# Kernel optimization log

Hardware: AMD Instinct MI355X
Metric: run time of the kernel (lower is better)

Reference implementation:

```python
import jax, jax.numpy as jnp
import numpy as np

W_NBITS = 8
A_NBITS = 8


def _fake_quant_weight_per_channel(w, nbits):
    # symmetric per-output-channel (row) fake quantization
    qmax = float(2 ** (nbits - 1) - 1)
    scale = jnp.max(jnp.abs(w), axis=1, keepdims=True) / qmax  # [out, 1]
    scale = jnp.maximum(scale, 1e-8)
    return jnp.clip(jnp.round(w / scale), -qmax - 1.0, qmax) * scale


def _fake_quant_act_per_group(x, group_size, nbits):
    # dynamic symmetric per-group fake quantization along the feature dim
    qmax = float(2 ** (nbits - 1) - 1)
    tokens, feat = x.shape
    xg = x.reshape(tokens, feat // group_size, group_size)
    scale = jnp.max(jnp.abs(xg), axis=-1, keepdims=True) / qmax  # [T, G, 1]
    scale = jnp.maximum(scale, 1e-8)
    xq = jnp.clip(jnp.round(xg / scale), -qmax - 1.0, qmax) * scale
    return xq.reshape(tokens, feat)


def setup_inputs() -> dict:
    key = jax.random.key(0)
    k1, k2, k3 = jax.random.split(key, 3)
    tokens, in_f, out_f = 8192, 4096, 4096
    x = jax.random.normal(k1, (tokens, in_f), dtype=jnp.float32)
    weight = jax.random.normal(k2, (out_f, in_f), dtype=jnp.float32) * 0.02
    bias = jax.random.normal(k3, (out_f,), dtype=jnp.float32) * 0.02
    return {"x": x, "weight": weight, "bias": bias, "group_size": 128}


def reference(x, weight, bias, group_size):
    w_q = _fake_quant_weight_per_channel(weight, W_NBITS)
    x_q = _fake_quant_act_per_group(x, group_size, A_NBITS)
    # F.linear: x @ w.T + b
    return jnp.einsum("tc,oc->to", x_q, w_q) + bias
```

## Files before the change

### kernel.cpp

```cpp
#include <hip/hip_runtime.h>
#include <stdint.h>


typedef __attribute__((ext_vector_type(4))) int   i32x4;
typedef __attribute__((ext_vector_type(4))) float f32x4;

static __device__ __forceinline__ void load_lds16(const void* g, void* l) {
    __builtin_amdgcn_global_load_lds(
        (const __attribute__((address_space(1))) void*)g,
        (__attribute__((address_space(3))) void*)l, 16, 0, 0);
}

static __device__ __forceinline__ int8_t q8m(float v, float inv) {
    float q = rintf(v * inv);
    q = fminf(fmaxf(q, -128.0f), 127.0f);
    return (int8_t)(int)q;
}

__global__ __launch_bounds__(256) void quant_act_kernel(
        const float* __restrict__ x, int8_t* __restrict__ xq,
        float* __restrict__ sxT, int M) {
    const int row = blockIdx.x, t = threadIdx.x;
    const float* xr = x + (size_t)row * 4096;
    float4 v[4];
#pragma unroll
    for (int i = 0; i < 4; i++)
        v[i] = *(const float4*)(xr + t * 16 + i * 4);
    float m = 0.0f;
#pragma unroll
    for (int i = 0; i < 4; i++)
        m = fmaxf(m, fmaxf(fmaxf(fabsf(v[i].x), fabsf(v[i].y)),
                           fmaxf(fabsf(v[i].z), fabsf(v[i].w))));
    m = fmaxf(m, __shfl_xor(m, 1));
    m = fmaxf(m, __shfl_xor(m, 2));
    m = fmaxf(m, __shfl_xor(m, 4));
    const float scale = fmaxf(m / 127.0f, 1e-8f);
    const float inv = 1.0f / scale;
    union { int8_t b[16]; i32x4 w; } o;
#pragma unroll
    for (int i = 0; i < 4; i++) {
        o.b[i * 4 + 0] = q8m(v[i].x, inv);
        o.b[i * 4 + 1] = q8m(v[i].y, inv);
        o.b[i * 4 + 2] = q8m(v[i].z, inv);
        o.b[i * 4 + 3] = q8m(v[i].w, inv);
    }
    *(i32x4*)(xq + (size_t)row * 4096 + t * 16) = o.w;
    if ((t & 7) == 0)
        sxT[(size_t)(t >> 3) * M + row] = scale;
}

__global__ __launch_bounds__(256) void quant_wgt_kernel(
        const float* __restrict__ w, int8_t* __restrict__ wq,
        float* __restrict__ sw) {
    const int row = blockIdx.x, t = threadIdx.x;
    const float* wr = w + (size_t)row * 4096;
    float4 v[4];
#pragma unroll
    for (int i = 0; i < 4; i++)
        v[i] = *(const float4*)(wr + t * 16 + i * 4);
    float m = 0.0f;
#pragma unroll
    for (int i = 0; i < 4; i++)
        m = fmaxf(m, fmaxf(fmaxf(fabsf(v[i].x), fabsf(v[i].y)),
                           fmaxf(fabsf(v[i].z), fabsf(v[i].w))));
#pragma unroll
    for (int off = 1; off < 64; off <<= 1)
        m = fmaxf(m, __shfl_xor(m, off));
    __shared__ float wm[4];
    if ((t & 63) == 0) wm[t >> 6] = m;
    __syncthreads();
    m = fmaxf(fmaxf(wm[0], wm[1]), fmaxf(wm[2], wm[3]));
    const float scale = fmaxf(m / 127.0f, 1e-8f);
    if (t == 0) sw[row] = scale;
    const float inv = 1.0f / scale;
    union { int8_t b[16]; i32x4 w4; } o;
#pragma unroll
    for (int i = 0; i < 4; i++) {
        o.b[i * 4 + 0] = q8m(v[i].x, inv);
        o.b[i * 4 + 1] = q8m(v[i].y, inv);
        o.b[i * 4 + 2] = q8m(v[i].z, inv);
        o.b[i * 4 + 3] = q8m(v[i].w, inv);
    }
    *(i32x4*)(wq + (size_t)row * 4096 + t * 16) = o.w4;
}

__global__ __launch_bounds__(256, 2) void gemm_i8_kernel(
        const int8_t* __restrict__ A, const int8_t* __restrict__ B,
        const float* __restrict__ sxT, const float* __restrict__ sw,
        const float* __restrict__ bias, float* __restrict__ C,
        int M, int N, int K) {
    __shared__ __align__(16) int8_t As[128 * 128];
    __shared__ __align__(16) int8_t Bs[128 * 128];
    const int tid = threadIdx.x;
    const int wave = tid >> 6, lane = tid & 63;
    const int bm = blockIdx.y * 128, bn = blockIdx.x * 128;
    const int wm = (wave >> 1) * 64, wn = (wave & 1) * 64;

    f32x4 acc[4][4];
#pragma unroll
    for (int i = 0; i < 4; i++)
#pragma unroll
        for (int j = 0; j < 4; j++) acc[i][j] = (f32x4){0.f, 0.f, 0.f, 0.f};

    const int srow = wave * 8 + (lane >> 3);
    const int scol = (((lane & 7) ^ ((lane >> 3) & 7)) * 16);
    const size_t sK = (size_t)K;
    const int8_t* Ag = A + (size_t)(bm + srow) * sK + scol;
    const int8_t* Bg = B + (size_t)(bn + srow) * sK + scol;
    int8_t* AsW = As + (wave * 8) * 128;
    int8_t* BsW = Bs + (wave * 8) * 128;

    const int fr = lane & 15, q = lane >> 4, r7 = lane & 7;
    const float* sxg = sxT + bm + wm + q * 4;

    for (int k0 = 0; k0 < K; k0 += 128) {
#pragma unroll
        for (int i = 0; i < 4; i++) {
            load_lds16(Ag + k0 + (size_t)i * 32 * sK, AsW + i * 32 * 128);
            load_lds16(Bg + k0 + (size_t)i * 32 * sK, BsW + i * 32 * 128);
        }
        f32x4 sxv[4];
#pragma unroll
        for (int mi = 0; mi < 4; mi++)
            sxv[mi] = *(const f32x4*)(sxg + (size_t)(k0 >> 7) * M + mi * 16);
        __syncthreads();

        i32x4 a[4][2], b[4][2];
#pragma unroll
        for (int mi = 0; mi < 4; mi++) {
            const int arow = wm + mi * 16 + fr;
            const int brow = wn + mi * 16 + fr;
#pragma unroll
            for (int h = 0; h < 2; h++) {
                a[mi][h] = *(const i32x4*)(As + arow * 128 +
                                           ((h * 4 + q) ^ r7) * 16);
                b[mi][h] = *(const i32x4*)(Bs + brow * 128 +
                                           ((h * 4 + q) ^ r7) * 16);
            }
        }
#pragma unroll
        for (int mi = 0; mi < 4; mi++)
#pragma unroll
            for (int ni = 0; ni < 4; ni++) {
                i32x4 iacc = __builtin_amdgcn_mfma_i32_16x16x64_i8(
                    a[mi][0], b[ni][0], (i32x4){0, 0, 0, 0}, 0, 0, 0);
                iacc = __builtin_amdgcn_mfma_i32_16x16x64_i8(
                    a[mi][1], b[ni][1], iacc, 0, 0, 0);
#pragma unroll
                for (int r = 0; r < 4; r++)
                    acc[mi][ni][r] += (float)iacc[r] * sxv[mi][r];
            }
        __syncthreads();
    }

    const int or0 = bm + wm + q * 4;
    const int oc0 = bn + wn + fr;
    float swv[4], bv[4];
#pragma unroll
    for (int ni = 0; ni < 4; ni++) {
        swv[ni] = sw[oc0 + ni * 16];
        bv[ni] = bias[oc0 + ni * 16];
    }
#pragma unroll
    for (int mi = 0; mi < 4; mi++)
#pragma unroll
        for (int ni = 0; ni < 4; ni++)
#pragma unroll
            for (int r = 0; r < 4; r++)
                C[(size_t)(or0 + mi * 16 + r) * N + (oc0 + ni * 16)] =
                    acc[mi][ni][r] * swv[ni] + bv[ni];
}

extern "C" void kernel_launch(void* const* d_in, const int* in_sizes, int n_in,
                              void* d_out, int out_size, void* d_ws, size_t ws_size,
                              hipStream_t stream) {
    const float* x    = (const float*)d_in[0];
    const float* w    = (const float*)d_in[1];
    const float* bias = (const float*)d_in[2];

    const int out_f  = in_sizes[2];
    const int in_f   = in_sizes[1] / out_f;
    const int tokens = in_sizes[0] / in_f;
    const int G = in_f / 128;

    int8_t* xq  = (int8_t*)d_ws;
    int8_t* wq  = xq + (size_t)tokens * in_f;
    float*  sxT = (float*)(wq + (size_t)out_f * in_f);
    float*  sw  = sxT + (size_t)G * tokens;
    float*  out = (float*)d_out;

    quant_act_kernel<<<tokens, 256, 0, stream>>>(x, xq, sxT, tokens);
    quant_wgt_kernel<<<out_f, 256, 0, stream>>>(w, wq, sw);

    dim3 grid(out_f / 128, tokens / 128);
    gemm_i8_kernel<<<grid, 256, 0, stream>>>(xq, wq, sxT, sw, bias, out,
                                             tokens, out_f, in_f);
}
```

Before: 445.8 us.

## Enlarge GEMM tile to 256x256 with double-buffered LDS ping-pong pipeline

Moves the int8 GEMM from 128x128 tiles with 4 waves to 256x256 tiles with 8 waves. The LDS tile buffers are double-buffered, and the global-to-LDS loads for the next K step are interleaved between four MFMA quadrants using explicit barriers, waitcnt and setprio. The workgroup index is remapped with an XCD-aware swizzle. The aim is to hide load latency and raise operand reuse. In exchange it uses 128KB of LDS per block, which limits occupancy, and it depends on fragile manual synchronisation.

```diff
diff --git a/kernel.cpp b/kernel.cpp
--- a/kernel.cpp
+++ b/kernel.cpp
@@ -84,74 +84,139 @@
     *(i32x4*)(wq + (size_t)row * 4096 + t * 16) = o.w4;
 }
 
-__global__ __launch_bounds__(256, 2) void gemm_i8_kernel(
+#define QUAD(mh, nh)                                                         \
+    _Pragma("unroll")                                                        \
+    for (int mi2 = 0; mi2 < 4; ++mi2) {                                      \
+        _Pragma("unroll")                                                    \
+        for (int nj = 0; nj < 2; ++nj) {                                     \
+            const int ni = (nh) * 2 + nj;                                    \
+            i32x4 t = __builtin_amdgcn_mfma_i32_16x16x64_i8(                 \
+                a[mi2][0], b[ni][0], (i32x4){0, 0, 0, 0}, 0, 0, 0);          \
+            t = __builtin_amdgcn_mfma_i32_16x16x64_i8(                       \
+                a[mi2][1], b[ni][1], t, 0, 0, 0);                            \
+            _Pragma("unroll")                                                \
+            for (int r = 0; r < 4; ++r)                                      \
+                acc[(mh) * 4 + mi2][ni][r] += (float)t[r] * sxv[mi2][r];     \
+        }                                                                    \
+    }
+
+__global__ __launch_bounds__(512, 2) void gemm_i8_kernel(
         const int8_t* __restrict__ A, const int8_t* __restrict__ B,
         const float* __restrict__ sxT, const float* __restrict__ sw,
         const float* __restrict__ bias, float* __restrict__ C,
         int M, int N, int K) {
-    __shared__ __align__(16) int8_t As[128 * 128];
-    __shared__ __align__(16) int8_t Bs[128 * 128];
+    __shared__ __align__(16) int8_t As[2][256 * 128];
+    __shared__ __align__(16) int8_t Bs[2][256 * 128];
     const int tid = threadIdx.x;
     const int wave = tid >> 6, lane = tid & 63;
-    const int bm = blockIdx.y * 128, bn = blockIdx.x * 128;
-    const int wm = (wave >> 1) * 64, wn = (wave & 1) * 64;
-
-    f32x4 acc[4][4];
-#pragma unroll
-    for (int i = 0; i < 4; i++)
-#pragma unroll
-        for (int j = 0; j < 4; j++) acc[i][j] = (f32x4){0.f, 0.f, 0.f, 0.f};
+
+    const int nwg = gridDim.x, nN = N >> 8;
+    const int wg = ((int)blockIdx.x & 7) * (nwg >> 3) + ((int)blockIdx.x >> 3);
+    const int bm = (wg / nN) << 8, bn = (wg % nN) << 8;
+
+    const int wm = (wave >> 2) << 7, wn = (wave & 3) << 6;
+    const int fr = lane & 15, q = lane >> 4, r7 = lane & 7;
 
     const int srow = wave * 8 + (lane >> 3);
-    const int scol = (((lane & 7) ^ ((lane >> 3) & 7)) * 16);
+    const int scol = ((lane & 7) ^ ((lane >> 3) & 7)) << 4;
     const size_t sK = (size_t)K;
     const int8_t* Ag = A + (size_t)(bm + srow) * sK + scol;
     const int8_t* Bg = B + (size_t)(bn + srow) * sK + scol;
-    int8_t* AsW = As + (wave * 8) * 128;
-    int8_t* BsW = Bs + (wave * 8) * 128;
-
-    const int fr = lane & 15, q = lane >> 4, r7 = lane & 7;
-    const float* sxg = sxT + bm + wm + q * 4;
-
-    for (int k0 = 0; k0 < K; k0 += 128) {
-#pragma unroll
-        for (int i = 0; i < 4; i++) {
-            load_lds16(Ag + k0 + (size_t)i * 32 * sK, AsW + i * 32 * 128);
-            load_lds16(Bg + k0 + (size_t)i * 32 * sK, BsW + i * 32 * 128);
+    const int sldsw = wave * 8 * 128;
+
+    f32x4 acc[8][4];
+#pragma unroll
+    for (int i = 0; i < 8; i++)
+#pragma unroll
+        for (int jn = 0; jn < 4; jn++) acc[i][jn] = (f32x4){0.f, 0.f, 0.f, 0.f};
+
+    const int abase = (wm + fr) * 128;
+    const int bbase = (wn + fr) * 128;
+    const int c0 = (q ^ r7) << 4, c1 = ((4 + q) ^ r7) << 4;
+    const float* sxw = sxT + bm + wm + q * 4;
+
+    const int NT = K >> 7;
+
+    load_lds16(Bg,             &Bs[0][sldsw]);
+    load_lds16(Bg +  64 * sK,  &Bs[0][ 64 * 128 + sldsw]);
+    load_lds16(Bg + 128 * sK,  &Bs[0][128 * 128 + sldsw]);
+    load_lds16(Bg + 192 * sK,  &Bs[0][192 * 128 + sldsw]);
+    load_lds16(Ag,             &As[0][sldsw]);
+    load_lds16(Ag + 128 * sK,  &As[0][128 * 128 + sldsw]);
+    load_lds16(Ag +  64 * sK,  &As[0][ 64 * 128 + sldsw]);
+    load_lds16(Ag + 192 * sK,  &As[0][192 * 128 + sldsw]);
+    asm volatile("s_waitcnt vmcnt(2)" ::: "memory");
+    __builtin_amdgcn_s_barrier();
+
+    for (int j = 0; j < NT; ++j) {
+        const int cur = j & 1, nxt = cur ^ 1;
+        const size_t kn = (size_t)((j + 1 < NT) ? j + 1 : j) << 7;
+        const int8_t* Ac = As[cur];
+        const int8_t* Bc = Bs[cur];
+        const float* sxg = sxw + (size_t)j * M;
+
+        i32x4 a[4][2], b[4][2];
+        f32x4 sxv[4];
+
+#pragma unroll
+        for (int i = 0; i < 4; ++i) {
+            a[i][0] = *(const i32x4*)(Ac + abase + i * 2048 + c0);
+            a[i][1] = *(const i32x4*)(Ac + abase + i * 2048 + c1);
+            b[i][0] = *(const i32x4*)(Bc + bbase + i * 2048 + c0);
+            b[i][1] = *(const i32x4*)(Bc + bbase + i * 2048 + c1);
         }
-        f32x4 sxv[4];
-#pragma unroll
-        for (int mi = 0; mi < 4; mi++)
-            sxv[mi] = *(const f32x4*)(sxg + (size_t)(k0 >> 7) * M + mi * 16);
-        __syncthreads();
-
-        i32x4 a[4][2], b[4][2];
-#pragma unroll
-        for (int mi = 0; mi < 4; mi++) {
-            const int arow = wm + mi * 16 + fr;
-            const int brow = wn + mi * 16 + fr;
-#pragma unroll
-            for (int h = 0; h < 2; h++) {
-                a[mi][h] = *(const i32x4*)(As + arow * 128 +
-                                           ((h * 4 + q) ^ r7) * 16);
-                b[mi][h] = *(const i32x4*)(Bs + brow * 128 +
-                                           ((h * 4 + q) ^ r7) * 16);
-            }
+#pragma unroll
+        for (int i = 0; i < 4; ++i)
+            sxv[i] = *(const f32x4*)(sxg + i * 16);
+        load_lds16(Bg + kn,            &Bs[nxt][sldsw]);
+        load_lds16(Bg + kn + 64 * sK,  &Bs[nxt][64 * 128 + sldsw]);
+        __builtin_amdgcn_s_barrier();
+        asm volatile("s_waitcnt lgkmcnt(0)" ::: "memory");
+        __builtin_amdgcn_sched_barrier(0);
+        __builtin_amdgcn_s_setprio(1);
+        QUAD(0, 0)
+        __builtin_amdgcn_s_setprio(0);
+        __builtin_amdgcn_s_barrier();
+
+        load_lds16(Bg + kn + 128 * sK, &Bs[nxt][128 * 128 + sldsw]);
+        load_lds16(Bg + kn + 192 * sK, &Bs[nxt][192 * 128 + sldsw]);
+        __builtin_amdgcn_s_barrier();
+        __builtin_amdgcn_sched_barrier(0);
+        __builtin_amdgcn_s_setprio(1);
+        QUAD(0, 1)
+        __builtin_amdgcn_s_setprio(0);
+        asm volatile("s_waitcnt vmcnt(4)" ::: "memory");
+        __builtin_amdgcn_s_barrier();
+
+#pragma unroll
+        for (int i = 0; i < 4; ++i) {
+            a[i][0] = *(const i32x4*)(Ac + abase + 64 * 128 + i * 2048 + c0);
+            a[i][1] = *(const i32x4*)(Ac + abase + 64 * 128 + i * 2048 + c1);
         }
 #pragma unroll
-        for (int mi = 0; mi < 4; mi++)
-#pragma unroll
-            for (int ni = 0; ni < 4; ni++) {
-                i32x4 iacc = __builtin_amdgcn_mfma_i32_16x16x64_i8(
-                    a[mi][0], b[ni][0], (i32x4){0, 0, 0, 0}, 0, 0, 0);
-                iacc = __builtin_amdgcn_mfma_i32_16x16x64_i8(
-                    a[mi][1], b[ni][1], iacc, 0, 0, 0);
-#pragma unroll
-                for (int r = 0; r < 4; r++)
-                    acc[mi][ni][r] += (float)iacc[r] * sxv[mi][r];
-            }
-        __syncthreads();
-    }
+        for (int i = 0; i < 4; ++i)
+            sxv[i] = *(const f32x4*)(sxg + 64 + i * 16);
+        load_lds16(Ag + kn,            &As[nxt][sldsw]);
+        load_lds16(Ag + kn + 128 * sK, &As[nxt][128 * 128 + sldsw]);
+        __builtin_amdgcn_s_barrier();
+        asm volatile("s_waitcnt lgkmcnt(0)" ::: "memory");
+        __builtin_amdgcn_sched_barrier(0);
+        __builtin_amdgcn_s_setprio(1);
+        QUAD(1, 0)
+        __builtin_amdgcn_s_setprio(0);
+        __builtin_amdgcn_s_barrier();
+
+        load_lds16(Ag + kn + 64 * sK,  &As[nxt][64 * 128 + sldsw]);
+        load_lds16(Ag + kn + 192 * sK, &As[nxt][192 * 128 + sldsw]);
+        __builtin_amdgcn_s_barrier();
+        __builtin_amdgcn_sched_barrier(0);
+        __builtin_amdgcn_s_setprio(1);
+        QUAD(1, 1)
+        __builtin_amdgcn_s_setprio(0);
+        asm volatile("s_waitcnt vmcnt(2)" ::: "memory");
+        __builtin_amdgcn_s_barrier();
+    }
+    asm volatile("s_waitcnt vmcnt(0)" ::: "memory");
 
     const int or0 = bm + wm + q * 4;
     const int oc0 = bn + wn + fr;
@@ -162,7 +227,7 @@
         bv[ni] = bias[oc0 + ni * 16];
     }
 #pragma unroll
-    for (int mi = 0; mi < 4; mi++)
+    for (int mi = 0; mi < 8; mi++)
 #pragma unroll
         for (int ni = 0; ni < 4; ni++)
 #pragma unroll
@@ -192,7 +257,7 @@
     quant_act_kernel<<<tokens, 256, 0, stream>>>(x, xq, sxT, tokens);
     quant_wgt_kernel<<<out_f, 256, 0, stream>>>(w, wq, sw);
 
-    dim3 grid(out_f / 128, tokens / 128);
-    gemm_i8_kernel<<<grid, 256, 0, stream>>>(xq, wq, sxT, sw, bias, out,
-                                             tokens, out_f, in_f);
-}
+    const int nwg = (tokens / 256) * (out_f / 256);
+    gemm_i8_kernel<<<nwg, 512, 0, stream>>>(xq, wq, sxT, sw, bias, out,
+                                            tokens, out_f, in_f);
+}
```

After: 475.4 us. 6.6% more time.

## Double-buffer LDS tiles with single barrier and XCD-aware block remap

Applied to the files above, without the earlier changes.

Switches the int8 GEMM to double-buffered LDS so the next K tile's global-to-LDS loads are issued while MFMAs run on the current tile. This cuts the loop to one barrier per iteration, guarded by an explicit vmcnt wait. It also replaces the 2D grid with a 1D grid remapped so consecutive blocks on the same XCD share tiles, aiming for better L2 reuse. Activation scales are prefetched one tile ahead into alternating registers. The cost is doubled LDS (64KB per block), which may hurt two-blocks-per-CU occupancy, and the loop assumes an even tile count.

```diff
diff --git a/kernel.cpp b/kernel.cpp
--- a/kernel.cpp
+++ b/kernel.cpp
@@ -84,74 +84,106 @@
     *(i32x4*)(wq + (size_t)row * 4096 + t * 16) = o.w4;
 }
 
+#define ITER(CUR, SXC, SXN, J)                                               \
+    {                                                                        \
+        asm volatile("s_waitcnt vmcnt(0)" ::: "memory");                     \
+        __builtin_amdgcn_s_barrier();                                        \
+        const int jn = ((J) + 1 < NT) ? (J) + 1 : (J);                       \
+        const size_t kn = (size_t)jn << 7;                                   \
+        load_lds16(Ag + kn,            &As[(CUR) ^ 1][sldsw]);               \
+        load_lds16(Ag + kn + 32 * sK,  &As[(CUR) ^ 1][32 * 128 + sldsw]);    \
+        load_lds16(Ag + kn + 64 * sK,  &As[(CUR) ^ 1][64 * 128 + sldsw]);    \
+        load_lds16(Ag + kn + 96 * sK,  &As[(CUR) ^ 1][96 * 128 + sldsw]);    \
+        load_lds16(Bg + kn,            &Bs[(CUR) ^ 1][sldsw]);               \
+        load_lds16(Bg + kn + 32 * sK,  &Bs[(CUR) ^ 1][32 * 128 + sldsw]);    \
+        load_lds16(Bg + kn + 64 * sK,  &Bs[(CUR) ^ 1][64 * 128 + sldsw]);    \
+        load_lds16(Bg + kn + 96 * sK,  &Bs[(CUR) ^ 1][96 * 128 + sldsw]);    \
+        _Pragma("unroll")                                                    \
+        for (int mi = 0; mi < 4; ++mi)                                       \
+            SXN[mi] = *(const f32x4*)(sxg + (size_t)jn * M + mi * 16);       \
+        i32x4 a[4][2], b[4][2];                                              \
+        _Pragma("unroll")                                                    \
+        for (int mi = 0; mi < 4; ++mi) {                                     \
+            const int arow = wm + mi * 16 + fr;                              \
+            const int brow = wn + mi * 16 + fr;                              \
+            _Pragma("unroll")                                                \
+            for (int h = 0; h < 2; ++h) {                                    \
+                a[mi][h] = *(const i32x4*)(As[CUR] + arow * 128 +            \
+                                           (((h * 4 + q) ^ r7) << 4));       \
+                b[mi][h] = *(const i32x4*)(Bs[CUR] + brow * 128 +            \
+                                           (((h * 4 + q) ^ r7) << 4));       \
+            }                                                                \
+        }                                                                    \
+        __builtin_amdgcn_sched_barrier(0);                                   \
+        _Pragma("unroll")                                                    \
+        for (int ni = 0; ni < 4; ++ni) {                                     \
+            i32x4 it[4];                                                     \
+            _Pragma("unroll")                                                \
+            for (int mi = 0; mi < 4; ++mi) {                                 \
+                it[mi] = __builtin_amdgcn_mfma_i32_16x16x64_i8(              \
+                    a[mi][0], b[ni][0], (i32x4){0, 0, 0, 0}, 0, 0, 0);       \
+                it[mi] = __builtin_amdgcn_mfma_i32_16x16x64_i8(              \
+                    a[mi][1], b[ni][1], it[mi], 0, 0, 0);                    \
+            }                                                                \
+            _Pragma("unroll")                                                \
+            for (int mi = 0; mi < 4; ++mi)                                   \
+                _Pragma("unroll")                                            \
+                for (int r = 0; r < 4; ++r)                                  \
+                    acc[mi][ni][r] += (float)it[mi][r] * SXC[mi][r];         \
+        }                                                                    \
+    }
+
 __global__ __launch_bounds__(256, 2) void gemm_i8_kernel(
         const int8_t* __restrict__ A, const int8_t* __restrict__ B,
         const float* __restrict__ sxT, const float* __restrict__ sw,
         const float* __restrict__ bias, float* __restrict__ C,
         int M, int N, int K) {
-    __shared__ __align__(16) int8_t As[128 * 128];
-    __shared__ __align__(16) int8_t Bs[128 * 128];
+    __shared__ __align__(16) int8_t As[2][128 * 128];
+    __shared__ __align__(16) int8_t Bs[2][128 * 128];
     const int tid = threadIdx.x;
     const int wave = tid >> 6, lane = tid & 63;
-    const int bm = blockIdx.y * 128, bn = blockIdx.x * 128;
-    const int wm = (wave >> 1) * 64, wn = (wave & 1) * 64;
-
-    f32x4 acc[4][4];
-#pragma unroll
-    for (int i = 0; i < 4; i++)
-#pragma unroll
-        for (int j = 0; j < 4; j++) acc[i][j] = (f32x4){0.f, 0.f, 0.f, 0.f};
+
+    const int nwg = gridDim.x, nN = N >> 7;
+    const int wg = ((int)blockIdx.x & 7) * (nwg >> 3) + ((int)blockIdx.x >> 3);
+    const int bm = (wg / nN) << 7, bn = (wg % nN) << 7;
+
+    const int wm = (wave >> 1) << 6, wn = (wave & 1) << 6;
+    const int fr = lane & 15, q = lane >> 4, r7 = lane & 7;
 
     const int srow = wave * 8 + (lane >> 3);
-    const int scol = (((lane & 7) ^ ((lane >> 3) & 7)) * 16);
+    const int scol = ((lane & 7) ^ ((lane >> 3) & 7)) << 4;
     const size_t sK = (size_t)K;
     const int8_t* Ag = A + (size_t)(bm + srow) * sK + scol;
     const int8_t* Bg = B + (size_t)(bn + srow) * sK + scol;
-    int8_t* AsW = As + (wave * 8) * 128;
-    int8_t* BsW = Bs + (wave * 8) * 128;
-
-    const int fr = lane & 15, q = lane >> 4, r7 = lane & 7;
+    const int sldsw = wave * 8 * 128;
+
+    f32x4 acc[4][4];
+#pragma unroll
+    for (int i = 0; i < 4; i++)
+#pragma unroll
+        for (int jn2 = 0; jn2 < 4; jn2++) acc[i][jn2] = (f32x4){0.f, 0.f, 0.f, 0.f};
+
     const float* sxg = sxT + bm + wm + q * 4;
-
-    for (int k0 = 0; k0 < K; k0 += 128) {
-#pragma unroll
-        for (int i = 0; i < 4; i++) {
-            load_lds16(Ag + k0 + (size_t)i * 32 * sK, AsW + i * 32 * 128);
-            load_lds16(Bg + k0 + (size_t)i * 32 * sK, BsW + i * 32 * 128);
-        }
-        f32x4 sxv[4];
-#pragma unroll
-        for (int mi = 0; mi < 4; mi++)
-            sxv[mi] = *(const f32x4*)(sxg + (size_t)(k0 >> 7) * M + mi * 16);
-        __syncthreads();
-
-        i32x4 a[4][2], b[4][2];
-#pragma unroll
-        for (int mi = 0; mi < 4; mi++) {
-            const int arow = wm + mi * 16 + fr;
-            const int brow = wn + mi * 16 + fr;
-#pragma unroll
-            for (int h = 0; h < 2; h++) {
-                a[mi][h] = *(const i32x4*)(As + arow * 128 +
-                                           ((h * 4 + q) ^ r7) * 16);
-                b[mi][h] = *(const i32x4*)(Bs + brow * 128 +
-                                           ((h * 4 + q) ^ r7) * 16);
-            }
-        }
-#pragma unroll
-        for (int mi = 0; mi < 4; mi++)
-#pragma unroll
-            for (int ni = 0; ni < 4; ni++) {
-                i32x4 iacc = __builtin_amdgcn_mfma_i32_16x16x64_i8(
-                    a[mi][0], b[ni][0], (i32x4){0, 0, 0, 0}, 0, 0, 0);
-                iacc = __builtin_amdgcn_mfma_i32_16x16x64_i8(
-                    a[mi][1], b[ni][1], iacc, 0, 0, 0);
-#pragma unroll
-                for (int r = 0; r < 4; r++)
-                    acc[mi][ni][r] += (float)iacc[r] * sxv[mi][r];
-            }
-        __syncthreads();
-    }
+    const int NT = K >> 7;
+
+    load_lds16(Ag,            &As[0][sldsw]);
+    load_lds16(Ag + 32 * sK,  &As[0][32 * 128 + sldsw]);
+    load_lds16(Ag + 64 * sK,  &As[0][64 * 128 + sldsw]);
+    load_lds16(Ag + 96 * sK,  &As[0][96 * 128 + sldsw]);
+    load_lds16(Bg,            &Bs[0][sldsw]);
+    load_lds16(Bg + 32 * sK,  &Bs[0][32 * 128 + sldsw]);
+    load_lds16(Bg + 64 * sK,  &Bs[0][64 * 128 + sldsw]);
+    load_lds16(Bg + 96 * sK,  &Bs[0][96 * 128 + sldsw]);
+    f32x4 sxa[4], sxb[4];
+#pragma unroll
+    for (int mi = 0; mi < 4; ++mi)
+        sxa[mi] = *(const f32x4*)(sxg + mi * 16);
+
+    for (int j = 0; j < NT; j += 2) {
+        ITER(0, sxa, sxb, j)
+        ITER(1, sxb, sxa, j + 1)
+    }
+    asm volatile("s_waitcnt vmcnt(0)" ::: "memory");
 
     const int or0 = bm + wm + q * 4;
     const int oc0 = bn + wn + fr;
@@ -192,7 +224,7 @@
     quant_act_kernel<<<tokens, 256, 0, stream>>>(x, xq, sxT, tokens);
     quant_wgt_kernel<<<out_f, 256, 0, stream>>>(w, wq, sw);
 
-    dim3 grid(out_f / 128, tokens / 128);
-    gemm_i8_kernel<<<grid, 256, 0, stream>>>(xq, wq, sxT, sw, bias, out,
-                                             tokens, out_f, in_f);
-}
+    const int nwg = (tokens / 128) * (out_f / 128);
+    gemm_i8_kernel<<<nwg, 256, 0, stream>>>(xq, wq, sxT, sw, bias, out,
+                                            tokens, out_f, in_f);
+}
```

After: 560.3 us. +25.7%, slower.

## Enlarge GEMM tile to 256 tokens and swap operands for vectorized stores

Applied to the files above, without the earlier changes.

The int8 GEMM block tile grows from 128x128 to 128 outputs by 256 tokens, with each wave computing a 64x128 sub-tile. Weights become the MFMA A operand and activations the B operand, so accumulator rows map to output channels. That lets the epilogue store with float4 writes and load scales and bias as vectors. The larger tile raises arithmetic intensity per LDS load, in exchange for twice the accumulator registers and 48KB of LDS, which may cut occupancy below two blocks per CU.

```diff
diff --git a/kernel.cpp b/kernel.cpp
--- a/kernel.cpp
+++ b/kernel.cpp
@@ -85,90 +85,107 @@
 }
 
 __global__ __launch_bounds__(256, 2) void gemm_i8_kernel(
-        const int8_t* __restrict__ A, const int8_t* __restrict__ B,
+        const int8_t* __restrict__ Xq, const int8_t* __restrict__ Wq,
         const float* __restrict__ sxT, const float* __restrict__ sw,
         const float* __restrict__ bias, float* __restrict__ C,
         int M, int N, int K) {
-    __shared__ __align__(16) int8_t As[128 * 128];
-    __shared__ __align__(16) int8_t Bs[128 * 128];
+    __shared__ __align__(16) int8_t Ws[128 * 128];
+    __shared__ __align__(16) int8_t Xs[256 * 128];
     const int tid = threadIdx.x;
     const int wave = tid >> 6, lane = tid & 63;
-    const int bm = blockIdx.y * 128, bn = blockIdx.x * 128;
-    const int wm = (wave >> 1) * 64, wn = (wave & 1) * 64;
-
-    f32x4 acc[4][4];
-#pragma unroll
-    for (int i = 0; i < 4; i++)
-#pragma unroll
-        for (int j = 0; j < 4; j++) acc[i][j] = (f32x4){0.f, 0.f, 0.f, 0.f};
+    const int bo = blockIdx.x * 128;
+    const int bt = blockIdx.y * 256;
+    const int wo = (wave & 1) << 6, wt = (wave >> 1) << 7;
+    const int fr = lane & 15, q = lane >> 4, r7 = lane & 7;
 
     const int srow = wave * 8 + (lane >> 3);
-    const int scol = (((lane & 7) ^ ((lane >> 3) & 7)) * 16);
+    const int scol = ((lane & 7) ^ ((lane >> 3) & 7)) << 4;
     const size_t sK = (size_t)K;
-    const int8_t* Ag = A + (size_t)(bm + srow) * sK + scol;
-    const int8_t* Bg = B + (size_t)(bn + srow) * sK + scol;
-    int8_t* AsW = As + (wave * 8) * 128;
-    int8_t* BsW = Bs + (wave * 8) * 128;
-
-    const int fr = lane & 15, q = lane >> 4, r7 = lane & 7;
-    const float* sxg = sxT + bm + wm + q * 4;
-
-    for (int k0 = 0; k0 < K; k0 += 128) {
-#pragma unroll
-        for (int i = 0; i < 4; i++) {
-            load_lds16(Ag + k0 + (size_t)i * 32 * sK, AsW + i * 32 * 128);
-            load_lds16(Bg + k0 + (size_t)i * 32 * sK, BsW + i * 32 * 128);
+    const int8_t* Wg = Wq + (size_t)(bo + srow) * sK + scol;
+    const int8_t* Xg = Xq + (size_t)(bt + srow) * sK + scol;
+    const int sldsw = wave * 8 * 128;
+
+    f32x4 facc[4][8];
+#pragma unroll
+    for (int i = 0; i < 4; i++)
+#pragma unroll
+        for (int jn = 0; jn < 8; jn++) facc[i][jn] = (f32x4){0.f, 0.f, 0.f, 0.f};
+
+    const float* sxb = sxT + bt + wt + fr;
+    const int NT = K >> 7;
+
+    for (int j = 0; j < NT; ++j) {
+        const size_t k0 = (size_t)j << 7;
+#pragma unroll
+        for (int i = 0; i < 4; ++i)
+            load_lds16(Wg + k0 + (size_t)i * 32 * sK, Ws + i * 32 * 128 + sldsw);
+#pragma unroll
+        for (int i = 0; i < 8; ++i)
+            load_lds16(Xg + k0 + (size_t)i * 32 * sK, Xs + i * 32 * 128 + sldsw);
+        float sxs[8];
+#pragma unroll
+        for (int ni = 0; ni < 8; ++ni)
+            sxs[ni] = sxb[(size_t)j * M + ni * 16];
+        __syncthreads();
+
+        i32x4 a[4][2];
+#pragma unroll
+        for (int mi = 0; mi < 4; ++mi) {
+            const int arow = (wo + mi * 16 + fr) * 128;
+#pragma unroll
+            for (int h = 0; h < 2; ++h)
+                a[mi][h] = *(const i32x4*)(Ws + arow + (((h * 4 + q) ^ r7) << 4));
         }
-        f32x4 sxv[4];
-#pragma unroll
-        for (int mi = 0; mi < 4; mi++)
-            sxv[mi] = *(const f32x4*)(sxg + (size_t)(k0 >> 7) * M + mi * 16);
-        __syncthreads();
-
-        i32x4 a[4][2], b[4][2];
-#pragma unroll
-        for (int mi = 0; mi < 4; mi++) {
-            const int arow = wm + mi * 16 + fr;
-            const int brow = wn + mi * 16 + fr;
-#pragma unroll
-            for (int h = 0; h < 2; h++) {
-                a[mi][h] = *(const i32x4*)(As + arow * 128 +
-                                           ((h * 4 + q) ^ r7) * 16);
-                b[mi][h] = *(const i32x4*)(Bs + brow * 128 +
-                                           ((h * 4 + q) ^ r7) * 16);
+#pragma unroll
+        for (int half = 0; half < 2; ++half) {
+            i32x4 b[4][2];
+#pragma unroll
+            for (int nj = 0; nj < 4; ++nj) {
+                const int brow = (wt + (half * 4 + nj) * 16 + fr) * 128;
+#pragma unroll
+                for (int h = 0; h < 2; ++h)
+                    b[nj][h] = *(const i32x4*)(Xs + brow +
+                                               (((h * 4 + q) ^ r7) << 4));
+            }
+#pragma unroll
+            for (int nj = 0; nj < 4; ++nj) {
+                const float s = sxs[half * 4 + nj];
+                i32x4 it[4];
+#pragma unroll
+                for (int mi = 0; mi < 4; ++mi) {
+                    it[mi] = __builtin_amdgcn_mfma_i32_16x16x64_i8(
+                        a[mi][0], b[nj][0], (i32x4){0, 0, 0, 0}, 0, 0, 0);
+                    it[mi] = __builtin_amdgcn_mfma_i32_16x16x64_i8(
+                        a[mi][1], b[nj][1], it[mi], 0, 0, 0);
+                }
+#pragma unroll
+                for (int mi = 0; mi < 4; ++mi)
+#pragma unroll
+                    for (int r = 0; r < 4; ++r)
+                        facc[mi][half * 4 + nj][r] += (float)it[mi][r] * s;
             }
         }
-#pragma unroll
-        for (int mi = 0; mi < 4; mi++)
-#pragma unroll
-            for (int ni = 0; ni < 4; ni++) {
-                i32x4 iacc = __builtin_amdgcn_mfma_i32_16x16x64_i8(
-                    a[mi][0], b[ni][0], (i32x4){0, 0, 0, 0}, 0, 0, 0);
-                iacc = __builtin_amdgcn_mfma_i32_16x16x64_i8(
-                    a[mi][1], b[ni][1], iacc, 0, 0, 0);
-#pragma unroll
-                for (int r = 0; r < 4; r++)
-                    acc[mi][ni][r] += (float)iacc[r] * sxv[mi][r];
-            }
         __syncthreads();
     }
 
-    const int or0 = bm + wm + q * 4;
-    const int oc0 = bn + wn + fr;
-    float swv[4], bv[4];
-#pragma unroll
-    for (int ni = 0; ni < 4; ni++) {
-        swv[ni] = sw[oc0 + ni * 16];
-        bv[ni] = bias[oc0 + ni * 16];
-    }
-#pragma unroll
-    for (int mi = 0; mi < 4; mi++)
-#pragma unroll
-        for (int ni = 0; ni < 4; ni++)
-#pragma unroll
-            for (int r = 0; r < 4; r++)
-                C[(size_t)(or0 + mi * 16 + r) * N + (oc0 + ni * 16)] =
-                    acc[mi][ni][r] * swv[ni] + bv[ni];
+    const int o4 = bo + wo + q * 4;
+    f32x4 swv[4], bv[4];
+#pragma unroll
+    for (int mi = 0; mi < 4; ++mi) {
+        swv[mi] = *(const f32x4*)(sw + o4 + mi * 16);
+        bv[mi]  = *(const f32x4*)(bias + o4 + mi * 16);
+    }
+#pragma unroll
+    for (int mi = 0; mi < 4; ++mi)
+#pragma unroll
+        for (int ni = 0; ni < 8; ++ni) {
+            f32x4 o;
+#pragma unroll
+            for (int r = 0; r < 4; ++r)
+                o[r] = facc[mi][ni][r] * swv[mi][r] + bv[mi][r];
+            const int t = bt + wt + ni * 16 + fr;
+            *(f32x4*)(C + (size_t)t * N + o4 + mi * 16) = o;
+        }
 }
 
 extern "C" void kernel_launch(void* const* d_in, const int* in_sizes, int n_in,
@@ -192,7 +209,7 @@
     quant_act_kernel<<<tokens, 256, 0, stream>>>(x, xq, sxT, tokens);
     quant_wgt_kernel<<<out_f, 256, 0, stream>>>(w, wq, sw);
 
-    dim3 grid(out_f / 128, tokens / 128);
+    dim3 grid(out_f / 128, tokens / 256);
     gemm_i8_kernel<<<grid, 256, 0, stream>>>(xq, wq, sxT, sw, bias, out,
                                              tokens, out_f, in_f);
 }
```

New measurement: 438.6 us. Within noise of the previous version (-1.6%).
